# Kernel optimization log

Hardware: AMD Instinct MI355X
Metric: run time of the kernel (lower is better)

Reference implementation:

```python
import jax, jax.numpy as jnp
import numpy as np

B, N = 16384, 31
N_INTS, N_OPS, N_PASSES = 10, 4, 4
NODE_LIT, NODE_OP = 0, 1


def setup_inputs() -> dict:
    key = jax.random.key(0)
    ks = jax.random.split(key, 7)
    cats = jax.random.randint(ks[0], (B, N), 0, 2)
    ops = jax.random.randint(ks[1], (B, N), 0, N_OPS)
    lits = jax.random.randint(ks[2], (B, N), 0, N_INTS)
    left = jax.random.randint(ks[3], (B, N), 0, N)
    right = jax.random.randint(ks[4], (B, N), 0, N)
    mask = jnp.ones((B, N), dtype=bool)
    op_table = jax.random.normal(ks[5], (N_OPS, N_INTS, N_INTS, N_INTS), dtype=jnp.float32) * 0.1
    return {"cats": cats, "ops": ops, "lits": lits, "left": left,
            "right": right, "mask": mask, "op_table": op_table}


def reference(cats, ops, lits, left, right, mask, op_table):
    left = jnp.clip(left, 0, N - 1)
    right = jnp.clip(right, 0, N - 1)
    ops_c = jnp.clip(ops, 0, N_OPS - 1)

    # init: literals -> one-hot over ints, everything else zero
    lit_mask = (cats == NODE_LIT) & mask                     # (B, N)
    lit_onehot = jax.nn.one_hot(jnp.clip(lits, 0, N_INTS - 1), N_INTS, dtype=jnp.float32)
    state = jnp.where(lit_mask[..., None], lit_onehot, 0.0)  # (B, N, n_ints)

    op_mask = (cats == NODE_OP) & mask
    brow = jnp.arange(B)[:, None]
    slice_table = op_table[ops_c]                             # (B, N, i, j, k)

    def op_step(state):
        left_dist = state[brow, left]                         # (B, N, n_ints)
        right_dist = state[brow, right]                       # (B, N, n_ints)
        logits = jnp.einsum('bni,bnj,bnijk->bnk', left_dist, right_dist, slice_table)
        dist = jax.nn.softmax(logits, axis=-1)
        new_state = jnp.where(op_mask[..., None], dist, state)
        return new_state, logits

    for _ in range(N_PASSES - 1):
        state, _ = op_step(state)
    state, node_logits = op_step(state)

    root_is_lit = (cats[:, 0] == NODE_LIT)[:, None].astype(jnp.float32)
    lit_logits = state[:, 0, :] * 10.0
    root_logits = root_is_lit * lit_logits + (1.0 - root_is_lit) * node_logits[:, 0, :]
    return root_logits
```

## Files before the change

kernel.cpp:

```cpp
#include <hip/hip_runtime.h>

#define NB 16384
#define NN 31
#define NI 10
#define NOPS 4
#define GB 64
#define TPB 1024
#define NWAVES 16
#define NPB (GB * NN)
#define ZSLOT (NPB + 10)
#define NROWS (NPB + 11)
#define NDR_TOT 1200
#define MAXT_PW 3
#define INVALID_NODE 0xFFFFu

typedef __attribute__((ext_vector_type(8))) short bf16x8_t;
typedef __attribute__((ext_vector_type(4))) float f32x4_t;

template <int CTRL>
__device__ __forceinline__ float dppf(float v) {
    return __int_as_float(__builtin_amdgcn_update_dpp(
        0, __float_as_int(v), CTRL, 0xF, 0xF, true));
}
__device__ __forceinline__ float rowsum16(float x) {
    x += dppf<0xB1>(x);
    x += dppf<0x4E>(x);
    x += dppf<0x124>(x);
    x += dppf<0x128>(x);
    return x;
}
__device__ __forceinline__ unsigned short f2bf(float f) {
    unsigned u = __float_as_uint(f);
    u += 0x7FFFu + ((u >> 16) & 1u);
    return (unsigned short)(u >> 16);
}
__device__ __forceinline__ unsigned cvtpk(float lo, float hi) {
    unsigned r;
    asm("v_cvt_pk_bf16_f32 %0, %1, %2" : "=v"(r) : "v"(lo), "v"(hi));
    return r;
}
__device__ __forceinline__ int ndrOff(int p) {
    return (p == 0) ? 0 : (p == 1) ? 572 : (p == 2) ? 888 : 1076;
}

__global__ __launch_bounds__(TPB, 4) void listops_mfma(
    const int* __restrict__ cats, const int* __restrict__ ops,
    const int* __restrict__ lits, const int* __restrict__ left,
    const int* __restrict__ right, const float* __restrict__ tbl,
    float* __restrict__ out)
{
    __shared__ __align__(16) float st[NROWS][12];
    __shared__ __align__(16) unsigned short Bl[NOPS * 4 * 64 * 8];
    __shared__ unsigned chLR[NPB];
    __shared__ unsigned short chIdx[NPB];
    __shared__ unsigned short slotOf[NPB];
    __shared__ unsigned opm[GB];
    __shared__ unsigned Mfr[4][GB];
    __shared__ unsigned short ndr[NDR_TOT];
    __shared__ int cntA[16], cntB[16], baseA[16], ntP[4];
    __shared__ unsigned char tOpA[4][36];

    const int tid = threadIdx.x;
    const int wv  = tid >> 6;
    const int l   = tid & 63;
    const int q   = l >> 4;
    const int c   = l & 15;

    float* tscr = &st[0][0];
    if (tid < 16) { cntA[tid] = 0; cntB[tid] = 0; }
    if (tid < GB) { opm[tid] = 0u; Mfr[0][tid] = 0u; Mfr[1][tid] = 0u; Mfr[2][tid] = 0u; }
    ndr[tid] = (unsigned short)INVALID_NODE;
    if (tid < NDR_TOT - TPB) ndr[TPB + tid] = (unsigned short)INVALID_NODE;
    if (tid < 132) {
        int r = tid / 12, k = tid - r * 12;
        st[NPB + r][k] = (r < NI && k == r) ? 1.0f : 0.0f;
    }
    if (tid < 1000) ((float4*)tscr)[tid] = ((const float4*)tbl)[tid];
    __syncthreads();

    {
        const int fi   = tid;
        const int lane = fi & 63;
        const int step = (fi >> 6) & 3;
        const int op   = fi >> 8;
        const int bq = lane >> 4, bn = lane & 15;
        unsigned short v[8];
        #pragma unroll
        for (int e = 0; e < 8; ++e) {
            float val = 0.0f;
            if (bn < NI) {
                if (step < 2) {
                    val = tscr[((op * NI + 4 * step + bq) * NI + e) * NI + bn];
                } else if (step == 2) {
                    if (bq < 2) val = tscr[((op * NI + 8 + bq) * NI + e) * NI + bn];
                } else {
                    if (bq < 2)      val = tscr[((op * NI + e) * NI + 8 + bq) * NI + bn];
                    else if (e < 2)  val = tscr[((op * NI + 8 + e) * NI + 8 + (bq - 2)) * NI + bn];
                }
            }
            v[e] = f2bf(val);
        }
        uint4 pk;
        pk.x = (unsigned)v[0] | ((unsigned)v[1] << 16);
        pk.y = (unsigned)v[2] | ((unsigned)v[3] << 16);
        pk.z = (unsigned)v[4] | ((unsigned)v[5] << 16);
        pk.w = (unsigned)v[6] | ((unsigned)v[7] << 16);
        ((uint4*)&Bl[0])[fi] = pk;
    }
    __syncthreads();

    #pragma unroll
    for (int rr = 0; rr < 2; ++rr) {
        int n = tid + rr * TPB;
        if (n < NPB) {
            int g   = blockIdx.x * NPB + n;
            int cat = cats[g];
            int op  = min(max(ops[g], 0), NOPS - 1);
            int lit = min(max(lits[g], 0), NI - 1);
            int b   = n / NN;
            int nl  = n - b * NN;
            int cl  = min(max(left[g],  0), NN - 1);
            int cr  = min(max(right[g], 0), NN - 1);
            chIdx[n]  = (unsigned short)(cl | (cr << 5) | (op << 10));
            slotOf[n] = (unsigned short)((cat == 0) ? (NPB + lit) : n);
            if (cat == 0) {
                if (nl == 0) {
                    float* o = out + (blockIdx.x * GB + b) * NI;
                    #pragma unroll
                    for (int k = 0; k < NI; ++k) o[k] = (k == lit) ? 10.0f : 0.0f;
                }
            } else {
                atomicOr(&opm[b], 1u << nl);
            }
        }
    }
    __syncthreads();

    #pragma unroll
    for (int rr = 0; rr < 2; ++rr) {
        int n = tid + rr * TPB;
        if (n < NPB) {
            int b  = n / NN;
            unsigned ch = chIdx[n];
            unsigned sl = slotOf[b * NN + (ch & 31)];
            unsigned sr = slotOf[b * NN + ((ch >> 5) & 31)];
            chLR[n] = (sl * 3u) | ((sr * 3u) << 16);
        }
    }
    if (tid < GB) Mfr[3][tid] = opm[tid] & 1u;
    __syncthreads();

    #pragma unroll
    for (int p = 3; p >= 1; --p) {
        #pragma unroll
        for (int rr = 0; rr < 2; ++rr) {
            int n = tid + rr * TPB;
            if (n < NPB) {
                int b  = n / NN;
                int nl = n - b * NN;
                if (((opm[b] >> nl) & 1u) && ((Mfr[p][b] >> nl) & 1u)) {
                    unsigned ch = chIdx[n];
                    atomicOr(&Mfr[p - 1][b], (1u << (ch & 31)) | (1u << ((ch >> 5) & 31)));
                }
            }
        }
        __syncthreads();
    }
    #pragma unroll
    for (int rr = 0; rr < 2; ++rr) {
        int n = tid + rr * TPB;
        if (n < NPB) {
            int b  = n / NN;
            int nl = n - b * NN;
            if ((opm[b] >> nl) & 1u) {
                int o = (chIdx[n] >> 10) & 3;
                #pragma unroll
                for (int p = 0; p < 4; ++p)
                    if ((Mfr[p][b] >> nl) & 1u) atomicAdd(&cntA[p * 4 + o], 1);
            }
        }
    }
    __syncthreads();
    if (tid == 0) {
        #pragma unroll
        for (int p = 0; p < 4; ++p) {
            int rb = 0, tc = 0;
            #pragma unroll
            for (int o = 0; o < NOPS; ++o) {
                baseA[p * 4 + o] = rb;
                int nt = (cntA[p * 4 + o] + 15) >> 4;
                for (int i = 0; i < nt; ++i) tOpA[p][tc++] = (unsigned char)o;
                rb += nt << 4;
            }
            ntP[p] = tc;
        }
    }
    __syncthreads();
    #pragma unroll
    for (int rr = 0; rr < 2; ++rr) {
        int n = tid + rr * TPB;
        if (n < NPB) {
            int b  = n / NN;
            int nl = n - b * NN;
            if ((opm[b] >> nl) & 1u) {
                int o = (chIdx[n] >> 10) & 3;
                #pragma unroll
                for (int p = 0; p < 4; ++p) {
                    if ((Mfr[p][b] >> nl) & 1u) {
                        int r = atomicAdd(&cntB[p * 4 + o], 1);
                        ndr[ndrOff(p) + baseA[p * 4 + o] + r] =
                            (unsigned short)((b << 5) | nl);
                    }
                }
            }
        }
    }
    __syncthreads();

    const char* sb = (const char*)&st[0][0];
    #pragma unroll 1
    for (int pass = 0; pass < 4; ++pass) {
        const unsigned short* nd = &ndr[ndrOff(pass)];
        const unsigned char* top = &tOpA[pass][0];
        const int nt = ntP[pass];
        f32x4_t acc[MAXT_PW];

        #pragma unroll
        for (int i = 0; i < MAXT_PW; ++i) {
            int t = wv + NWAVES * i;
            if (t < nt) {
                int rowv = nd[t * 16 + c];
                int idx  = (rowv == (int)INVALID_NODE) ? 0
                         : ((rowv >> 5) * NN + (rowv & 31));
                unsigned lrp = chLR[idx];
                if (pass == 0) {
                    unsigned lo = lrp & 0xFFFFu, hi = lrp >> 16;
                    lo = (lo < 3u * NPB) ? (3u * ZSLOT) : lo;
                    hi = (hi < 3u * NPB) ? (3u * ZSLOT) : hi;
                    lrp = lo | (hi << 16);
                }
                const char* Lb = sb + ((lrp & 0xFFFFu) << 4);
                const char* Rb = sb + ((lrp >> 16) << 4);
                float4 l0  = *(const float4*)Lb;
                float4 l1  = *(const float4*)(Lb + 16);
                float2 l89 = *(const float2*)(Lb + 32);
                float4 r0  = *(const float4*)Rb;
                float4 r1  = *(const float4*)(Rb + 16);
                float2 r89 = *(const float2*)(Rb + 32);

                float lq0 = (q & 2) ? ((q & 1) ? l0.w : l0.z) : ((q & 1) ? l0.y : l0.x);
                float lq1 = (q & 2) ? ((q & 1) ? l1.w : l1.z) : ((q & 1) ? l1.y : l1.x);
                float lq2 = (q == 0) ? l89.x : ((q == 1) ? l89.y : 0.0f);

                float Re[8] = {r0.x, r0.y, r0.z, r0.w, r1.x, r1.y, r1.z, r1.w};
                float Le[8] = {l0.x, l0.y, l0.z, l0.w, l1.x, l1.y, l1.z, l1.w};

                bf16x8_t av0, av1, av2, av3;
                unsigned* a0 = (unsigned*)&av0;
                unsigned* a1 = (unsigned*)&av1;
                unsigned* a2 = (unsigned*)&av2;
                unsigned* a3 = (unsigned*)&av3;
                float rsel = (q & 1) ? r89.y : r89.x;
                const bool qlo = (q < 2);
                float w3[8];
                w3[0] = (qlo ? Le[0] : l89.x) * rsel;
                w3[1] = (qlo ? Le[1] : l89.y) * rsel;
                #pragma unroll
                for (int e = 2; e < 8; ++e) w3[e] = (qlo ? Le[e] : 0.0f) * rsel;
                #pragma unroll
                for (int d = 0; d < 4; ++d) {
                    a0[d] = cvtpk(lq0 * Re[2 * d], lq0 * Re[2 * d + 1]);
                    a1[d] = cvtpk(lq1 * Re[2 * d], lq1 * Re[2 * d + 1]);
                    a2[d] = cvtpk(lq2 * Re[2 * d], lq2 * Re[2 * d + 1]);
                    a3[d] = cvtpk(w3[2 * d], w3[2 * d + 1]);
                }

                const char* Bp = (const char*)&Bl[0] + (int)top[t] * 4096 + l * 16;
                f32x4_t a = {0.0f, 0.0f, 0.0f, 0.0f};
                a = __builtin_amdgcn_mfma_f32_16x16x32_bf16(av0, *(const bf16x8_t*)(Bp + 0 * 1024), a, 0, 0, 0);
                a = __builtin_amdgcn_mfma_f32_16x16x32_bf16(av1, *(const bf16x8_t*)(Bp + 1 * 1024), a, 0, 0, 0);
                a = __builtin_amdgcn_mfma_f32_16x16x32_bf16(av2, *(const bf16x8_t*)(Bp + 2 * 1024), a, 0, 0, 0);
                a = __builtin_amdgcn_mfma_f32_16x16x32_bf16(av3, *(const bf16x8_t*)(Bp + 3 * 1024), a, 0, 0, 0);
                acc[i] = a;
            }
        }
        __syncthreads();

        if (pass < 3) {
            #pragma unroll
            for (int i = 0; i < MAXT_PW; ++i) {
                int t = wv + NWAVES * i;
                if (t < nt) {
                    f32x4_t a = acc[i];
                    ushort4 nds = *(const ushort4*)&nd[t * 16 + 4 * q];
                    const unsigned short* np = (const unsigned short*)&nds;
                    #pragma unroll
                    for (int r = 0; r < 4; ++r) {
                        float ex = (c < NI) ? __expf(a[r]) : 0.0f;
                        float sd = rowsum16(ex);
                        float pv = ex * __builtin_amdgcn_rcpf(sd);
                        unsigned short ndv = np[r];
                        if (ndv != (unsigned short)INVALID_NODE && c < NI) {
                            int i2 = ((int)ndv >> 5) * NN + ((int)ndv & 31);
                            st[i2][c] = pv;
                        }
                    }
                }
            }
            __syncthreads();
        } else {
            #pragma unroll
            for (int i = 0; i < MAXT_PW; ++i) {
                int t = wv + NWAVES * i;
                if (t < nt) {
                    f32x4_t a = acc[i];
                    ushort4 nds = *(const ushort4*)&nd[t * 16 + 4 * q];
                    const unsigned short* np = (const unsigned short*)&nds;
                    #pragma unroll
                    for (int r = 0; r < 4; ++r) {
                        unsigned short ndv = np[r];
                        if (ndv != (unsigned short)INVALID_NODE && c < NI) {
                            int b = (int)ndv >> 5;
                            out[(blockIdx.x * GB + b) * NI + c] = a[r];
                        }
                    }
                }
            }
        }
    }
}

extern "C" void kernel_launch(void* const* d_in, const int* in_sizes, int n_in,
                              void* d_out, int out_size, void* d_ws, size_t ws_size,
                              hipStream_t stream) {
    const int*   cats     = (const int*)  d_in[0];
    const int*   ops      = (const int*)  d_in[1];
    const int*   lits     = (const int*)  d_in[2];
    const int*   left     = (const int*)  d_in[3];
    const int*   right    = (const int*)  d_in[4];
    const float* op_table = (const float*)d_in[6];
    float*       out      = (float*)      d_out;

    hipLaunchKernelGGL(listops_mfma, dim3(NB / GB), dim3(TPB), 0, stream,
                       cats, ops, lits, left, right, op_table, out);
}
```

Baseline: 17.01 us.

## Prefetch inputs early, fold counting into frontier passes, parallelize tile scan

Global loads of node inputs and the op table are issued at kernel start so their latency overlaps the LDS setup and table repacking. The chIdx/slotOf setup is merged into the same phase as the B-matrix repacking, removing one barrier. Per-pass op counting moves into the frontier-propagation loop, and pass 3's frontier is seeded directly from root nodes. The serial single-thread prefix scan becomes a 16-thread computation. Together these cut barriers and serial work in the setup preamble, at the cost of more live registers and slightly more complex indexing.

```diff
diff --git a/kernel.cpp b/kernel.cpp
--- a/kernel.cpp
+++ b/kernel.cpp
@@ -66,6 +66,14 @@
     const int q   = l >> 4;
     const int c   = l & 15;
 
+    const int g0 = blockIdx.x * NPB + tid;
+    const bool v1 = (tid + TPB) < NPB;
+    const int g1 = v1 ? (g0 + TPB) : g0;
+    int cat0 = cats[g0], opv0 = ops[g0], lit0 = lits[g0], lf0 = left[g0], rt0 = right[g0];
+    int cat1 = cats[g1], opv1 = ops[g1], lit1 = lits[g1], lf1 = left[g1], rt1 = right[g1];
+    float4 tv = make_float4(0.f, 0.f, 0.f, 0.f);
+    if (tid < 1000) tv = ((const float4*)tbl)[tid];
+
     float* tscr = &st[0][0];
     if (tid < 16) { cntA[tid] = 0; cntB[tid] = 0; }
     if (tid < GB) { opm[tid] = 0u; Mfr[0][tid] = 0u; Mfr[1][tid] = 0u; Mfr[2][tid] = 0u; }
@@ -75,7 +83,7 @@
         int r = tid / 12, k = tid - r * 12;
         st[NPB + r][k] = (r < NI && k == r) ? 1.0f : 0.0f;
     }
-    if (tid < 1000) ((float4*)tscr)[tid] = ((const float4*)tbl)[tid];
+    if (tid < 1000) ((float4*)tscr)[tid] = tv;
     __syncthreads();
 
     {
@@ -107,51 +115,86 @@
         pk.w = (unsigned)v[6] | ((unsigned)v[7] << 16);
         ((uint4*)&Bl[0])[fi] = pk;
     }
+    int myOp0 = 0, myCl0 = 0, myCr0 = 0;
+    {
+        int n = tid;
+        int b  = n / NN, nl = n - b * NN;
+        myOp0 = min(max(opv0, 0), NOPS - 1);
+        int lit = min(max(lit0, 0), NI - 1);
+        myCl0 = min(max(lf0, 0), NN - 1);
+        myCr0 = min(max(rt0, 0), NN - 1);
+        chIdx[n]  = (unsigned short)(myCl0 | (myCr0 << 5) | (myOp0 << 10));
+        slotOf[n] = (unsigned short)((cat0 == 0) ? (NPB + lit) : n);
+        if (cat0 == 0) {
+            if (nl == 0) {
+                float* o = out + (blockIdx.x * GB + b) * NI;
+                #pragma unroll
+                for (int k = 0; k < NI; ++k) o[k] = (k == lit) ? 10.0f : 0.0f;
+            }
+        } else {
+            atomicOr(&opm[b], 1u << nl);
+        }
+        if (v1) {
+            n = tid + TPB;
+            b = n / NN; nl = n - b * NN;
+            int op  = min(max(opv1, 0), NOPS - 1);
+            int li  = min(max(lit1, 0), NI - 1);
+            int cl  = min(max(lf1, 0), NN - 1);
+            int cr  = min(max(rt1, 0), NN - 1);
+            chIdx[n]  = (unsigned short)(cl | (cr << 5) | (op << 10));
+            slotOf[n] = (unsigned short)((cat1 == 0) ? (NPB + li) : n);
+            if (cat1 == 0) {
+                if (nl == 0) {
+                    float* o = out + (blockIdx.x * GB + b) * NI;
+                    #pragma unroll
+                    for (int k = 0; k < NI; ++k) o[k] = (k == li) ? 10.0f : 0.0f;
+                }
+            } else {
+                atomicOr(&opm[b], 1u << nl);
+            }
+        }
+    }
     __syncthreads();
 
     #pragma unroll
     for (int rr = 0; rr < 2; ++rr) {
         int n = tid + rr * TPB;
         if (n < NPB) {
-            int g   = blockIdx.x * NPB + n;
-            int cat = cats[g];
-            int op  = min(max(ops[g], 0), NOPS - 1);
-            int lit = min(max(lits[g], 0), NI - 1);
-            int b   = n / NN;
-            int nl  = n - b * NN;
-            int cl  = min(max(left[g],  0), NN - 1);
-            int cr  = min(max(right[g], 0), NN - 1);
-            chIdx[n]  = (unsigned short)(cl | (cr << 5) | (op << 10));
-            slotOf[n] = (unsigned short)((cat == 0) ? (NPB + lit) : n);
-            if (cat == 0) {
-                if (nl == 0) {
-                    float* o = out + (blockIdx.x * GB + b) * NI;
-                    #pragma unroll
-                    for (int k = 0; k < NI; ++k) o[k] = (k == lit) ? 10.0f : 0.0f;
-                }
-            } else {
-                atomicOr(&opm[b], 1u << nl);
-            }
-        }
-    }
-    __syncthreads();
-
-    #pragma unroll
-    for (int rr = 0; rr < 2; ++rr) {
-        int n = tid + rr * TPB;
-        if (n < NPB) {
-            int b  = n / NN;
+            int b = n / NN;
             unsigned ch = chIdx[n];
             unsigned sl = slotOf[b * NN + (ch & 31)];
             unsigned sr = slotOf[b * NN + ((ch >> 5) & 31)];
             chLR[n] = (sl * 3u) | ((sr * 3u) << 16);
         }
     }
-    if (tid < GB) Mfr[3][tid] = opm[tid] & 1u;
+    {
+        int b = tid / NN, nl = tid - (tid / NN) * NN;
+        if (nl == 0) {
+            unsigned isop = opm[b] & 1u;
+            Mfr[3][b] = isop;
+            if (isop) {
+                atomicOr(&Mfr[2][b], (1u << myCl0) | (1u << myCr0));
+                atomicAdd(&cntA[12 + myOp0], 1);
+            }
+        }
+        if (v1) {
+            int n = tid + TPB;
+            int b2 = n / NN, nl2 = n - b2 * NN;
+            if (nl2 == 0) {
+                unsigned isop = opm[b2] & 1u;
+                Mfr[3][b2] = isop;
+                if (isop) {
+                    unsigned ch = chIdx[n];
+                    atomicOr(&Mfr[2][b2], (1u << (ch & 31)) | (1u << ((ch >> 5) & 31)));
+                    atomicAdd(&cntA[12 + ((ch >> 10) & 3)], 1);
+                }
+            }
+        }
+    }
     __syncthreads();
 
     #pragma unroll
-    for (int p = 3; p >= 1; --p) {
+    for (int p = 2; p >= 1; --p) {
         #pragma unroll
         for (int rr = 0; rr < 2; ++rr) {
             int n = tid + rr * TPB;
@@ -161,6 +204,7 @@
                 if (((opm[b] >> nl) & 1u) && ((Mfr[p][b] >> nl) & 1u)) {
                     unsigned ch = chIdx[n];
                     atomicOr(&Mfr[p - 1][b], (1u << (ch & 31)) | (1u << ((ch >> 5) & 31)));
+                    atomicAdd(&cntA[p * 4 + ((ch >> 10) & 3)], 1);
                 }
             }
         }
@@ -172,30 +216,26 @@
         if (n < NPB) {
             int b  = n / NN;
             int nl = n - b * NN;
-            if ((opm[b] >> nl) & 1u) {
-                int o = (chIdx[n] >> 10) & 3;
-                #pragma unroll
-                for (int p = 0; p < 4; ++p)
-                    if ((Mfr[p][b] >> nl) & 1u) atomicAdd(&cntA[p * 4 + o], 1);
-            }
-        }
-    }
-    __syncthreads();
-    if (tid == 0) {
-        #pragma unroll
-        for (int p = 0; p < 4; ++p) {
-            int rb = 0, tc = 0;
-            #pragma unroll
-            for (int o = 0; o < NOPS; ++o) {
-                baseA[p * 4 + o] = rb;
-                int nt = (cntA[p * 4 + o] + 15) >> 4;
-                for (int i = 0; i < nt; ++i) tOpA[p][tc++] = (unsigned char)o;
-                rb += nt << 4;
-            }
-            ntP[p] = tc;
-        }
-    }
-    __syncthreads();
+            if (((opm[b] >> nl) & 1u) && ((Mfr[0][b] >> nl) & 1u))
+                atomicAdd(&cntA[(chIdx[n] >> 10) & 3], 1);
+        }
+    }
+    __syncthreads();
+
+    if (tid < 16) {
+        int p = tid >> 2, o = tid & 3;
+        int nt0 = (cntA[p * 4 + 0] + 15) >> 4;
+        int nt1 = (cntA[p * 4 + 1] + 15) >> 4;
+        int nt2 = (cntA[p * 4 + 2] + 15) >> 4;
+        int nt3 = (cntA[p * 4 + 3] + 15) >> 4;
+        int myNt = (o == 0) ? nt0 : (o == 1) ? nt1 : (o == 2) ? nt2 : nt3;
+        int tb = ((o > 0) ? nt0 : 0) + ((o > 1) ? nt1 : 0) + ((o > 2) ? nt2 : 0);
+        baseA[p * 4 + o] = tb << 4;
+        for (int i = 0; i < myNt; ++i) tOpA[p][tb + i] = (unsigned char)o;
+        if (o == 3) ntP[p] = tb + nt3;
+    }
+    __syncthreads();
+
     #pragma unroll
     for (int rr = 0; rr < 2; ++rr) {
         int n = tid + rr * TPB;
```

After: 15.20 us. 10.7% less time.
